# Optimization experiments

Hardware: AMD Instinct MI355X
Metric: run time of the kernel (lower is better)

Reference implementation:

```python
import jax, jax.numpy as jnp
import numpy as np

KS = 8        # hardcoded kernel size in MWPT
FIL_LEN = 8   # chosen filter length (db4-style), so pad pl = 0


def _transform_matrix():
    # mat[row, idx] = (-1)**idx for idx = KS-1 .. 0, scaled by (-1)**(FIL_LEN//2)
    mat = np.zeros((KS, KS), dtype=np.float32)
    for row, idx in enumerate(range(KS - 1, -1, -1)):
        mat[row, idx] = (-1.0) ** idx
    mat *= (-1.0) ** (FIL_LEN // 2)
    return jnp.asarray(mat)


def setup_inputs() -> dict:
    key = jax.random.key(0)
    k1, k2 = jax.random.split(key)
    x = jax.random.normal(k1, (128, 1, 65536), dtype=jnp.float32)
    kernel = jax.random.normal(k2, (1, 1, KS), dtype=jnp.float32)
    return {"x": x, "kernel": kernel}


def _conv(x, w):
    # circular pad (ks//2-1, ks//2-1) then stride-2 cross-correlation, halves T
    xp = jnp.pad(x, ((0, 0), (0, 0), (KS // 2 - 1, KS // 2 - 1)), mode='wrap')
    return jax.lax.conv_general_dilated(
        xp, w, window_strides=(2,), padding='VALID',
        dimension_numbers=('NCH', 'OIH', 'NCH'))


def _fwd(x, kernel):
    mat = _transform_matrix()
    k_lo = kernel                                   # low-pass
    k_hi = jnp.einsum('oik,kj->oij', kernel, mat)   # kernel @ mat, high-pass QMF
    # level 1: node 0 -> (0 low, 4 high)
    a0 = _conv(x, k_lo)
    a4 = _conv(x, k_hi)
    # level 2: 0->(0,2), 4->(4,6)
    b0 = _conv(a0, k_lo); b2 = _conv(a0, k_hi)
    b4 = _conv(a4, k_lo); b6 = _conv(a4, k_hi)
    # level 3: 0->(0,1), 2->(2,3), 4->(4,5), 6->(6,7)
    c0 = _conv(b0, k_lo); c1 = _conv(b0, k_hi)
    c2 = _conv(b2, k_lo); c3 = _conv(b2, k_hi)
    c4 = _conv(b4, k_lo); c5 = _conv(b4, k_hi)
    c6 = _conv(b6, k_lo); c7 = _conv(b6, k_hi)
    # forward() compacts each level's list then reindexes with gray code i^(i>>1)
    level1 = jnp.stack([a0, a4], axis=2)                       # [B,1,2,T/2]
    level2 = jnp.stack([b0, b2, b6, b4], axis=2)               # gray of [b0,b2,b4,b6]
    level3 = jnp.stack([c0, c1, c3, c2, c6, c7, c5, c4], axis=2)  # gray of c0..c7
    return level1, level2, level3


def reference(x, kernel):
    return _fwd(x, kernel)
```

## Files before the change

### kernel.cpp

```cpp
#include <hip/hip_runtime.h>


#define T_MASK  65535
#define PAD(i)  ((i) + ((i) >> 3))

#define XS_N 2090
#define AS_N 1042
#define BS_N 518
#define XS_P (PAD(XS_N - 1) + 1)
#define AS_P (PAD(AS_N - 1) + 1)
#define BS_P (PAD(BS_N - 1) + 1)

__global__ __launch_bounds__(256) void mwpt_kernel(
    const float* __restrict__ x, const float* __restrict__ ker,
    float* __restrict__ out)
{
    __shared__ float lds[XS_P + 2 * AS_P];
    float* xs  = lds;
    float* as0 = lds + XS_P;
    float* as1 = lds + XS_P + AS_P;
    float* bs0 = lds;
    float* bs1 = lds + BS_P;
    float* bs2 = lds + 2 * BS_P;
    float* bs3 = lds + 3 * BS_P;

    const int t   = threadIdx.x;
    const int seg = blockIdx.x;
    const int bi  = blockIdx.y;
    const int N3  = seg * 256;
    const int N2  = seg * 512;
    const int N1  = seg * 1024;
    const float* __restrict__ xrow = x + (size_t)bi * 65536;

    const int xg0 = 2 * N1 - 21;
    for (int i = t; i < XS_N; i += 256)
        xs[PAD(i)] = xrow[(xg0 + i) & T_MASK];

    float lo[8], hi[8];
#pragma unroll
    for (int k = 0; k < 8; ++k) lo[k] = ker[k];
#pragma unroll
    for (int k = 0; k < 8; ++k) hi[k] = (k & 1) ? -ker[7 - k] : ker[7 - k];

    __syncthreads();

    {
        const int j0 = 4 * t + 9;
        float xv[14];
#pragma unroll
        for (int q = 0; q < 14; ++q) xv[q] = xs[PAD(2 * j0 + q)];
        float r0[4], r4[4];
#pragma unroll
        for (int i = 0; i < 4; ++i) {
            float s0 = 0.f, s4 = 0.f;
#pragma unroll
            for (int k = 0; k < 8; ++k) {
                float v = xv[2 * i + k];
                s0 += v * lo[k]; s4 += v * hi[k];
            }
            r0[i] = s0; r4[i] = s4;
        }
#pragma unroll
        for (int i = 0; i < 4; ++i) {
            as0[PAD(j0 + i)] = r0[i];
            as1[PAD(j0 + i)] = r4[i];
        }
        if (t < 18) {
            int j = (t < 9) ? t : (1024 + t);
            float s0 = 0.f, s4 = 0.f;
#pragma unroll
            for (int k = 0; k < 8; ++k) {
                float v = xs[PAD(2 * j + k)];
                s0 += v * lo[k]; s4 += v * hi[k];
            }
            as0[PAD(j)] = s0; as1[PAD(j)] = s4;
        }
        size_t o = (size_t)bi * 65536 + (size_t)N1 + 4 * (size_t)t;
        *(float4*)(out + o)         = make_float4(r0[0], r0[1], r0[2], r0[3]);
        *(float4*)(out + o + 32768) = make_float4(r4[0], r4[1], r4[2], r4[3]);
    }

    __syncthreads();

    {
        const int m0 = 2 * t + 3;
        float av0[10], av1[10];
#pragma unroll
        for (int q = 0; q < 10; ++q) {
            av0[q] = as0[PAD(2 * m0 + q)];
            av1[q] = as1[PAD(2 * m0 + q)];
        }
        float v0[2], v2[2], v4[2], v6[2];
#pragma unroll
        for (int j = 0; j < 2; ++j) {
            float s0 = 0.f, s2 = 0.f, s4 = 0.f, s6 = 0.f;
#pragma unroll
            for (int k = 0; k < 8; ++k) {
                float a0 = av0[2 * j + k], a4 = av1[2 * j + k];
                s0 += a0 * lo[k]; s2 += a0 * hi[k];
                s4 += a4 * lo[k]; s6 += a4 * hi[k];
            }
            v0[j] = s0; v2[j] = s2; v4[j] = s4; v6[j] = s6;
        }
#pragma unroll
        for (int j = 0; j < 2; ++j) {
            bs0[PAD(m0 + j)] = v0[j];
            bs1[PAD(m0 + j)] = v2[j];
            bs2[PAD(m0 + j)] = v4[j];
            bs3[PAD(m0 + j)] = v6[j];
        }
        if (t < 6) {
            int m = (t < 3) ? t : (512 + t);
            float s0 = 0.f, s2 = 0.f, s4 = 0.f, s6 = 0.f;
#pragma unroll
            for (int k = 0; k < 8; ++k) {
                float a0 = as0[PAD(2 * m + k)], a4 = as1[PAD(2 * m + k)];
                s0 += a0 * lo[k]; s2 += a0 * hi[k];
                s4 += a4 * lo[k]; s6 += a4 * hi[k];
            }
            bs0[PAD(m)] = s0; bs1[PAD(m)] = s2;
            bs2[PAD(m)] = s4; bs3[PAD(m)] = s6;
        }
        size_t o = 8388608ull + (size_t)bi * 65536 + (size_t)N2 + 2 * (size_t)t;
        *(float2*)(out + o)             = make_float2(v0[0], v0[1]);
        *(float2*)(out + o + 16384)     = make_float2(v2[0], v2[1]);
        *(float2*)(out + o + 2 * 16384) = make_float2(v6[0], v6[1]);
        *(float2*)(out + o + 3 * 16384) = make_float2(v4[0], v4[1]);
    }

    __syncthreads();

    {
        float c0 = 0.f, c1 = 0.f, c2 = 0.f, c3 = 0.f;
        float c4 = 0.f, c5 = 0.f, c6 = 0.f, c7 = 0.f;
#pragma unroll
        for (int k = 0; k < 8; ++k) {
            float b0 = bs0[PAD(2 * t + k)];
            float b2 = bs1[PAD(2 * t + k)];
            float b4 = bs2[PAD(2 * t + k)];
            float b6 = bs3[PAD(2 * t + k)];
            c0 += b0 * lo[k]; c1 += b0 * hi[k];
            c2 += b2 * lo[k]; c3 += b2 * hi[k];
            c4 += b4 * lo[k]; c5 += b4 * hi[k];
            c6 += b6 * lo[k]; c7 += b6 * hi[k];
        }
        size_t o = 16777216ull + (size_t)bi * 65536 + (size_t)N3 + (size_t)t;
        out[o]            = c0;
        out[o + 8192]     = c1;
        out[o + 2 * 8192] = c3;
        out[o + 3 * 8192] = c2;
        out[o + 4 * 8192] = c6;
        out[o + 5 * 8192] = c7;
        out[o + 6 * 8192] = c5;
        out[o + 7 * 8192] = c4;
    }
}

extern "C" void kernel_launch(void* const* d_in, const int* in_sizes, int n_in,
                              void* d_out, int out_size, void* d_ws, size_t ws_size,
                              hipStream_t stream) {
    const float* x   = (const float*)d_in[0];
    const float* ker = (const float*)d_in[1];
    float* out = (float*)d_out;
    dim3 grid(32, 128), block(256);
    hipLaunchKernelGGL(mwpt_kernel, grid, block, 0, stream, x, ker, out);
}
```

Baseline: 131.0 us.

## Double per-block segment size with float4 input loads and wider per-thread outputs

Each block now covers twice as many samples (grid halved to 16x128), so the halo recomputed per block is amortised over more output. Global input loads become float4, and every level writes wider vector stores (float4 and float2). The LDS padding changes from every 8 to every 16 floats. In exchange the kernel uses more LDS and registers per thread, which may lower occupancy, and there are half as many blocks to spread across the CUs.

```diff
diff --git a/kernel.cpp b/kernel.cpp
--- a/kernel.cpp
+++ b/kernel.cpp
@@ -1,15 +1,15 @@
 #include <hip/hip_runtime.h>
 
 
-#define T_MASK  65535
-#define PAD(i)  ((i) + ((i) >> 3))
+#define T_MASK 65535
+#define P(i)   ((i) + ((i) >> 4))
 
-#define XS_N 2090
-#define AS_N 1042
-#define BS_N 518
-#define XS_P (PAD(XS_N - 1) + 1)
-#define AS_P (PAD(AS_N - 1) + 1)
-#define BS_P (PAD(BS_N - 1) + 1)
+#define XS_N 4144
+#define AS_N 2066
+#define BS_N 1030
+#define XS_P (P(XS_N - 1) + 1)
+#define AS_P (P(AS_N - 1) + 1)
+#define BS_P (P(BS_N - 1) + 1)
 
 __global__ __launch_bounds__(256) void mwpt_kernel(
     const float* __restrict__ x, const float* __restrict__ ker,
@@ -27,14 +27,18 @@
     const int t   = threadIdx.x;
     const int seg = blockIdx.x;
     const int bi  = blockIdx.y;
-    const int N3  = seg * 256;
-    const int N2  = seg * 512;
-    const int N1  = seg * 1024;
+    const int N1  = seg * 2048;
+    const int N2  = seg * 1024;
+    const int N3  = seg * 512;
     const float* __restrict__ xrow = x + (size_t)bi * 65536;
 
-    const int xg0 = 2 * N1 - 21;
-    for (int i = t; i < XS_N; i += 256)
-        xs[PAD(i)] = xrow[(xg0 + i) & T_MASK];
+    const int A = 4096 * seg - 24;
+    for (int u = t; u < 1036; u += 256) {
+        int g = (A + 4 * u) & T_MASK;
+        float4 v = *(const float4*)(xrow + g);
+        int ip = P(4 * u);
+        xs[ip] = v.x; xs[ip + 1] = v.y; xs[ip + 2] = v.z; xs[ip + 3] = v.w;
+    }
 
     float lo[8], hi[8];
 #pragma unroll
@@ -45,13 +49,12 @@
     __syncthreads();
 
     {
-        const int j0 = 4 * t + 9;
-        float xv[14];
+        float xv[22];
 #pragma unroll
-        for (int q = 0; q < 14; ++q) xv[q] = xs[PAD(2 * j0 + q)];
-        float r0[4], r4[4];
+        for (int q = 0; q < 22; ++q) xv[q] = xs[P(16 * t + 21 + q)];
+        float r0[8], r4[8];
 #pragma unroll
-        for (int i = 0; i < 4; ++i) {
+        for (int i = 0; i < 8; ++i) {
             float s0 = 0.f, s4 = 0.f;
 #pragma unroll
             for (int k = 0; k < 8; ++k) {
@@ -61,98 +64,110 @@
             r0[i] = s0; r4[i] = s4;
         }
 #pragma unroll
-        for (int i = 0; i < 4; ++i) {
-            as0[PAD(j0 + i)] = r0[i];
-            as1[PAD(j0 + i)] = r4[i];
+        for (int i = 0; i < 8; ++i) {
+            as0[P(8 * t + 9 + i)] = r0[i];
+            as1[P(8 * t + 9 + i)] = r4[i];
         }
         if (t < 18) {
-            int j = (t < 9) ? t : (1024 + t);
+            int jj = (t < 9) ? t : (2048 + t);
             float s0 = 0.f, s4 = 0.f;
 #pragma unroll
             for (int k = 0; k < 8; ++k) {
-                float v = xs[PAD(2 * j + k)];
+                float v = xs[P(2 * jj + 3 + k)];
                 s0 += v * lo[k]; s4 += v * hi[k];
             }
-            as0[PAD(j)] = s0; as1[PAD(j)] = s4;
+            as0[P(jj)] = s0; as1[P(jj)] = s4;
         }
-        size_t o = (size_t)bi * 65536 + (size_t)N1 + 4 * (size_t)t;
-        *(float4*)(out + o)         = make_float4(r0[0], r0[1], r0[2], r0[3]);
-        *(float4*)(out + o + 32768) = make_float4(r4[0], r4[1], r4[2], r4[3]);
+        size_t o = (size_t)bi * 65536 + (size_t)N1 + 8 * (size_t)t;
+        *(float4*)(out + o)             = make_float4(r0[0], r0[1], r0[2], r0[3]);
+        *(float4*)(out + o + 4)         = make_float4(r0[4], r0[5], r0[6], r0[7]);
+        *(float4*)(out + o + 32768)     = make_float4(r4[0], r4[1], r4[2], r4[3]);
+        *(float4*)(out + o + 32768 + 4) = make_float4(r4[4], r4[5], r4[6], r4[7]);
     }
 
     __syncthreads();
 
     {
-        const int m0 = 2 * t + 3;
-        float av0[10], av1[10];
+        float av0[14], av1[14];
 #pragma unroll
-        for (int q = 0; q < 10; ++q) {
-            av0[q] = as0[PAD(2 * m0 + q)];
-            av1[q] = as1[PAD(2 * m0 + q)];
+        for (int q = 0; q < 14; ++q) {
+            av0[q] = as0[P(8 * t + 6 + q)];
+            av1[q] = as1[P(8 * t + 6 + q)];
         }
-        float v0[2], v2[2], v4[2], v6[2];
+        float v0[4], v2[4], v4[4], v6[4];
 #pragma unroll
-        for (int j = 0; j < 2; ++j) {
+        for (int i = 0; i < 4; ++i) {
             float s0 = 0.f, s2 = 0.f, s4 = 0.f, s6 = 0.f;
 #pragma unroll
             for (int k = 0; k < 8; ++k) {
-                float a0 = av0[2 * j + k], a4 = av1[2 * j + k];
+                float a0 = av0[2 * i + k], a4 = av1[2 * i + k];
                 s0 += a0 * lo[k]; s2 += a0 * hi[k];
                 s4 += a4 * lo[k]; s6 += a4 * hi[k];
             }
-            v0[j] = s0; v2[j] = s2; v4[j] = s4; v6[j] = s6;
+            v0[i] = s0; v2[i] = s2; v4[i] = s4; v6[i] = s6;
         }
 #pragma unroll
-        for (int j = 0; j < 2; ++j) {
-            bs0[PAD(m0 + j)] = v0[j];
-            bs1[PAD(m0 + j)] = v2[j];
-            bs2[PAD(m0 + j)] = v4[j];
-            bs3[PAD(m0 + j)] = v6[j];
+        for (int i = 0; i < 4; ++i) {
+            int m = 4 * t + 3 + i;
+            bs0[P(m)] = v0[i]; bs1[P(m)] = v2[i];
+            bs2[P(m)] = v4[i]; bs3[P(m)] = v6[i];
         }
         if (t < 6) {
-            int m = (t < 3) ? t : (512 + t);
+            int m = (t < 3) ? t : (1024 + t);
             float s0 = 0.f, s2 = 0.f, s4 = 0.f, s6 = 0.f;
 #pragma unroll
             for (int k = 0; k < 8; ++k) {
-                float a0 = as0[PAD(2 * m + k)], a4 = as1[PAD(2 * m + k)];
+                float a0 = as0[P(2 * m + k)], a4 = as1[P(2 * m + k)];
                 s0 += a0 * lo[k]; s2 += a0 * hi[k];
                 s4 += a4 * lo[k]; s6 += a4 * hi[k];
             }
-            bs0[PAD(m)] = s0; bs1[PAD(m)] = s2;
-            bs2[PAD(m)] = s4; bs3[PAD(m)] = s6;
+            bs0[P(m)] = s0; bs1[P(m)] = s2;
+            bs2[P(m)] = s4; bs3[P(m)] = s6;
         }
-        size_t o = 8388608ull + (size_t)bi * 65536 + (size_t)N2 + 2 * (size_t)t;
-        *(float2*)(out + o)             = make_float2(v0[0], v0[1]);
-        *(float2*)(out + o + 16384)     = make_float2(v2[0], v2[1]);
-        *(float2*)(out + o + 2 * 16384) = make_float2(v6[0], v6[1]);
-        *(float2*)(out + o + 3 * 16384) = make_float2(v4[0], v4[1]);
+        size_t o = 8388608ull + (size_t)bi * 65536 + (size_t)N2 + 4 * (size_t)t;
+        *(float4*)(out + o)             = make_float4(v0[0], v0[1], v0[2], v0[3]);
+        *(float4*)(out + o + 16384)     = make_float4(v2[0], v2[1], v2[2], v2[3]);
+        *(float4*)(out + o + 2 * 16384) = make_float4(v6[0], v6[1], v6[2], v6[3]);
+        *(float4*)(out + o + 3 * 16384) = make_float4(v4[0], v4[1], v4[2], v4[3]);
     }
 
     __syncthreads();
 
     {
-        float c0 = 0.f, c1 = 0.f, c2 = 0.f, c3 = 0.f;
-        float c4 = 0.f, c5 = 0.f, c6 = 0.f, c7 = 0.f;
+        float bv0[10], bv1[10], bv2[10], bv3[10];
 #pragma unroll
-        for (int k = 0; k < 8; ++k) {
-            float b0 = bs0[PAD(2 * t + k)];
-            float b2 = bs1[PAD(2 * t + k)];
-            float b4 = bs2[PAD(2 * t + k)];
-            float b6 = bs3[PAD(2 * t + k)];
-            c0 += b0 * lo[k]; c1 += b0 * hi[k];
-            c2 += b2 * lo[k]; c3 += b2 * hi[k];
-            c4 += b4 * lo[k]; c5 += b4 * hi[k];
-            c6 += b6 * lo[k]; c7 += b6 * hi[k];
+        for (int q = 0; q < 10; ++q) {
+            bv0[q] = bs0[P(4 * t + q)];
+            bv1[q] = bs1[P(4 * t + q)];
+            bv2[q] = bs2[P(4 * t + q)];
+            bv3[q] = bs3[P(4 * t + q)];
         }
-        size_t o = 16777216ull + (size_t)bi * 65536 + (size_t)N3 + (size_t)t;
-        out[o]            = c0;
-        out[o + 8192]     = c1;
-        out[o + 2 * 8192] = c3;
-        out[o + 3 * 8192] = c2;
-        out[o + 4 * 8192] = c6;
-        out[o + 5 * 8192] = c7;
-        out[o + 6 * 8192] = c5;
-        out[o + 7 * 8192] = c4;
+        float c0[2], c1[2], c2[2], c3[2], c4[2], c5[2], c6[2], c7[2];
+#pragma unroll
+        for (int j = 0; j < 2; ++j) {
+            float s0 = 0.f, s1 = 0.f, s2 = 0.f, s3 = 0.f;
+            float s4 = 0.f, s5 = 0.f, s6 = 0.f, s7 = 0.f;
+#pragma unroll
+            for (int k = 0; k < 8; ++k) {
+                float b0 = bv0[2 * j + k], b2 = bv1[2 * j + k];
+                float b4 = bv2[2 * j + k], b6 = bv3[2 * j + k];
+                s0 += b0 * lo[k]; s1 += b0 * hi[k];
+                s2 += b2 * lo[k]; s3 += b2 * hi[k];
+                s4 += b4 * lo[k]; s5 += b4 * hi[k];
+                s6 += b6 * lo[k]; s7 += b6 * hi[k];
+            }
+            c0[j] = s0; c1[j] = s1; c2[j] = s2; c3[j] = s3;
+            c4[j] = s4; c5[j] = s5; c6[j] = s6; c7[j] = s7;
+        }
+        size_t o = 16777216ull + (size_t)bi * 65536 + (size_t)N3 + 2 * (size_t)t;
+        *(float2*)(out + o)            = make_float2(c0[0], c0[1]);
+        *(float2*)(out + o + 8192)     = make_float2(c1[0], c1[1]);
+        *(float2*)(out + o + 2 * 8192) = make_float2(c3[0], c3[1]);
+        *(float2*)(out + o + 3 * 8192) = make_float2(c2[0], c2[1]);
+        *(float2*)(out + o + 4 * 8192) = make_float2(c6[0], c6[1]);
+        *(float2*)(out + o + 5 * 8192) = make_float2(c7[0], c7[1]);
+        *(float2*)(out + o + 6 * 8192) = make_float2(c5[0], c5[1]);
+        *(float2*)(out + o + 7 * 8192) = make_float2(c4[0], c4[1]);
     }
 }
 
@@ -162,6 +177,6 @@
     const float* x   = (const float*)d_in[0];
     const float* ker = (const float*)d_in[1];
     float* out = (float*)d_out;
-    dim3 grid(32, 128), block(256);
+    dim3 grid(16, 128), block(256);
     hipLaunchKernelGGL(mwpt_kernel, grid, block, 0, stream, x, ker, out);
 }
```

New measurement: 129.7 us. No clear change (-1.0%).
